# Kernel optimization log

Hardware: AMD Instinct MI355X
Metric: run time of the kernel (lower is better)

Reference implementation:

```python
import jax, jax.numpy as jnp
import numpy as np

B, S, E, H = 4, 2048, 1024, 16
HD = E // H  # head_dim = 64


def setup_inputs() -> dict:
    key = jax.random.key(0)
    ks = jax.random.split(key, 9)
    s_in = 1.0 / np.sqrt(E)
    return {
        "x": jax.random.normal(ks[0], (B, S, E), dtype=jnp.float32),
        "Wq": jax.random.normal(ks[1], (E, E), dtype=jnp.float32) * s_in,
        "bq": jax.random.normal(ks[2], (E,), dtype=jnp.float32) * 0.01,
        "Wk": jax.random.normal(ks[3], (E, E), dtype=jnp.float32) * s_in,
        "bk": jax.random.normal(ks[4], (E,), dtype=jnp.float32) * 0.01,
        "Wv": jax.random.normal(ks[5], (E, E), dtype=jnp.float32) * s_in,
        "bv": jax.random.normal(ks[6], (E,), dtype=jnp.float32) * 0.01,
        "Wo": jax.random.normal(ks[7], (E, E), dtype=jnp.float32) * s_in,
        "bo": jax.random.normal(ks[8], (E,), dtype=jnp.float32) * 0.01,
    }


def reference(x, Wq, bq, Wk, bk, Wv, bv, Wo, bo):
    b, s, e = x.shape
    # fused QKV projections (equivalent to concatenated per-head linears)
    q = x @ Wq + bq  # [b, s, e]
    k = x @ Wk + bk
    v = x @ Wv + bv
    # split heads: [b, h, s, hd]
    def split(t):
        return t.reshape(b, s, H, HD).transpose(0, 2, 1, 3)
    q, k, v = split(q), split(k), split(v)
    scale = 1.0 / np.sqrt(HD)
    attn = jnp.einsum("bhqd,bhkd->bhqk", q, k) * scale  # [b, h, s, s]
    causal = jnp.tril(jnp.ones((s, s), dtype=bool))
    attn = jnp.where(causal[None, None], attn, -jnp.inf)
    attn = jax.nn.softmax(attn, axis=-1)
    y = jnp.einsum("bhqk,bhkd->bhqd", attn, v)  # [b, h, s, hd]
    y = y.transpose(0, 2, 1, 3).reshape(b, s, e)
    return y @ Wo + bo
```

## Files before the change

kernel.cpp:

```cpp
#include <hip/hip_runtime.h>
#include <hip/hip_bf16.h>

#define B_ 4
#define S_ 2048
#define E_ 1024
#define H_ 16
#define HD_ 64
#define QS 3072

typedef __attribute__((ext_vector_type(8))) short bf16x8;
typedef __attribute__((ext_vector_type(4))) float f32x4;

__device__ __forceinline__ float b2f(unsigned short u) {
    union { unsigned u; float f; } v; v.u = ((unsigned)u) << 16; return v.f;
}
__device__ __forceinline__ unsigned short f2b(float f) {
    union { float f; unsigned u; } v; v.f = f;
    unsigned lsb = (v.u >> 16) & 1u;
    v.u += 0x7fffu + lsb;
    return (unsigned short)(v.u >> 16);
}
__device__ __forceinline__ unsigned cvtpk_bf16(float lo, float hi) {
    unsigned r;
    asm("v_cvt_pk_bf16_f32 %0, %1, %2" : "=v"(r) : "v"(lo), "v"(hi));
    return r;
}

typedef const __attribute__((address_space(1))) unsigned glb_u32;
typedef __attribute__((address_space(3))) unsigned lds_u32;
__device__ __forceinline__ void gl_lds16(const unsigned short* g,
                                         unsigned short* l) {
    __builtin_amdgcn_global_load_lds((glb_u32*)g, (lds_u32*)l, 16, 0, 0);
}

__global__ void cvt_f32_to_bf16(const float* __restrict__ in,
                                unsigned short* __restrict__ out, int n8) {
    int i = blockIdx.x * blockDim.x + threadIdx.x;
    if (i >= n8) return;
    const float4* p = (const float4*)(in + (size_t)i * 8);
    float4 a = p[0], b = p[1];
    bf16x8 o;
    o[0] = (short)f2b(a.x); o[1] = (short)f2b(a.y);
    o[2] = (short)f2b(a.z); o[3] = (short)f2b(a.w);
    o[4] = (short)f2b(b.x); o[5] = (short)f2b(b.y);
    o[6] = (short)f2b(b.z); o[7] = (short)f2b(b.w);
    *(bf16x8*)(out + (size_t)i * 8) = o;
}

__global__ void transpose_cvt4(const float* __restrict__ W0,
                               const float* __restrict__ W1,
                               const float* __restrict__ W2,
                               const float* __restrict__ W3,
                               unsigned short* __restrict__ Wqkv,
                               unsigned short* __restrict__ Wto) {
    __shared__ float tile[32][33];
    int z = blockIdx.z;
    const float* W = (z == 0) ? W0 : (z == 1) ? W1 : (z == 2) ? W2 : W3;
    unsigned short* Wt = (z < 3) ? Wqkv + (size_t)z * 1024 * E_ : Wto;
    int tx = threadIdx.x, ty = threadIdx.y;
    int x0 = blockIdx.x * 32, y0 = blockIdx.y * 32;
#pragma unroll
    for (int j = 0; j < 32; j += 8)
        tile[ty + j][tx] = W[(size_t)(y0 + ty + j) * E_ + x0 + tx];
    __syncthreads();
#pragma unroll
    for (int j = 0; j < 32; j += 8)
        Wt[(size_t)(x0 + ty + j) * E_ + y0 + tx] = f2b(tile[tx][ty + j]);
}

#define BM 128
#define BN 128
#define BK 32

__global__ __launch_bounds__(256) void gemm_bt(
        const unsigned short* __restrict__ A,
        const unsigned short* __restrict__ Bt,
        const float* __restrict__ b0, const float* __restrict__ b1,
        const float* __restrict__ b2,
        unsigned short* __restrict__ Cb,
        int M, int N, int K) {
    __shared__ unsigned short As[BM][BK];
    __shared__ unsigned short Bs[BN][BK];
    int t = threadIdx.x;
    int lane = t & 63, wid = t >> 6;
    int wr = wid >> 1, wc = wid & 1;
    int nwg = gridDim.x * gridDim.y;
    int bid = blockIdx.y * gridDim.x + blockIdx.x;
    int ti = (bid & 7) * (nwg >> 3) + (bid >> 3);
    int bx = ti % gridDim.x, by = ti / gridDim.x;
    const int row = t >> 2, kc = (t & 3) << 3;
    const unsigned short* ga0 = A + (size_t)(by * BM + row) * K + kc;
    const unsigned short* gb0 = Bt + (size_t)(bx * BN + row) * K + kc;
    unsigned short* la0 = &As[0][0] + (size_t)t * 8;
    unsigned short* lb0 = &Bs[0][0] + (size_t)t * 8;
    const size_t step64 = (size_t)64 * K;

    f32x4 acc[4][4] = {};

    for (int ko = 0; ko < K; ko += BK) {
        gl_lds16(ga0 + ko, la0);
        gl_lds16(ga0 + ko + step64, la0 + 2048);
        gl_lds16(gb0 + ko, lb0);
        gl_lds16(gb0 + ko + step64, lb0 + 2048);
        __syncthreads();
        int kg = (lane >> 4) << 3;
        bf16x8 af[4], bfr[4];
#pragma unroll
        for (int i = 0; i < 4; ++i) {
            af[i]  = *(const bf16x8*)&As[wr * 64 + i * 16 + (lane & 15)][kg];
            bfr[i] = *(const bf16x8*)&Bs[wc * 64 + i * 16 + (lane & 15)][kg];
        }
#pragma unroll
        for (int i = 0; i < 4; ++i)
#pragma unroll
            for (int j = 0; j < 4; ++j)
                acc[i][j] = __builtin_amdgcn_mfma_f32_16x16x32_bf16(
                    af[i], bfr[j], acc[i][j], 0, 0, 0);
        __syncthreads();
    }

#pragma unroll
    for (int i = 0; i < 4; ++i) {
        int row0 = by * BM + wr * 64 + i * 16 + ((lane >> 4) << 2);
#pragma unroll
        for (int j = 0; j < 4; ++j) {
            int col = bx * BN + wc * 64 + j * 16 + (lane & 15);
            const float* bp = (col < 1024) ? b0 : ((col < 2048) ? b1 : b2);
            float bv = bp[col & 1023];
#pragma unroll
            for (int r = 0; r < 4; ++r) {
                int rr = row0 + r;
                Cb[(size_t)rr * N + col] = f2b(acc[i][j][r] + bv);
            }
        }
    }
}

__global__ __launch_bounds__(256) void gemm_bt_out(
        const unsigned short* __restrict__ A,
        const unsigned short* __restrict__ Bt,
        const float* __restrict__ bias,
        float* __restrict__ Cf, int M, int N, int K) {
    __shared__ unsigned short As[64][BK];
    __shared__ unsigned short Bs[BN][BK];
    int t = threadIdx.x;
    int lane = t & 63, wid = t >> 6;
    int wr = wid >> 1, wc = wid & 1;
    int nwg = gridDim.x * gridDim.y;
    int bid = blockIdx.y * gridDim.x + blockIdx.x;
    int ti = (bid & 7) * (nwg >> 3) + (bid >> 3);
    int bx = ti % gridDim.x, by = ti / gridDim.x;
    const int row = t >> 2, kc = (t & 3) << 3;
    const unsigned short* ga0 = A + (size_t)(by * 64 + row) * K + kc;
    const unsigned short* gb0 = Bt + (size_t)(bx * BN + row) * K + kc;
    unsigned short* la0 = &As[0][0] + (size_t)t * 8;
    unsigned short* lb0 = &Bs[0][0] + (size_t)t * 8;
    const size_t step64 = (size_t)64 * K;

    f32x4 acc[2][4] = {};

    for (int ko = 0; ko < K; ko += BK) {
        gl_lds16(ga0 + ko, la0);
        gl_lds16(gb0 + ko, lb0);
        gl_lds16(gb0 + ko + step64, lb0 + 2048);
        __syncthreads();
        int kg = (lane >> 4) << 3;
        bf16x8 af[2], bfr[4];
#pragma unroll
        for (int i = 0; i < 2; ++i)
            af[i] = *(const bf16x8*)&As[wr * 32 + i * 16 + (lane & 15)][kg];
#pragma unroll
        for (int j = 0; j < 4; ++j)
            bfr[j] = *(const bf16x8*)&Bs[wc * 64 + j * 16 + (lane & 15)][kg];
#pragma unroll
        for (int i = 0; i < 2; ++i)
#pragma unroll
            for (int j = 0; j < 4; ++j)
                acc[i][j] = __builtin_amdgcn_mfma_f32_16x16x32_bf16(
                    af[i], bfr[j], acc[i][j], 0, 0, 0);
        __syncthreads();
    }

#pragma unroll
    for (int i = 0; i < 2; ++i) {
        int row0 = by * 64 + wr * 32 + i * 16 + ((lane >> 4) << 2);
#pragma unroll
        for (int j = 0; j < 4; ++j) {
            int col = bx * BN + wc * 64 + j * 16 + (lane & 15);
            float bv = bias[col];
#pragma unroll
            for (int r = 0; r < 4; ++r)
                Cf[(size_t)(row0 + r) * N + col] = acc[i][j][r] + bv;
        }
    }
}

#define KVBLK 64

__global__ __launch_bounds__(256) void attn_mfma(
        const unsigned short* __restrict__ QKV,
        unsigned short* __restrict__ Yb) {
    __shared__ unsigned short Ks[2][KVBLK][64];
    __shared__ unsigned short Vt[2][64][KVBLK];
    __shared__ unsigned short Pl[4][16][64];

    int t = threadIdx.x;
    int lane = t & 63, wid = t >> 6;
    int l15 = lane & 15, lg = lane >> 4;
    int bh = blockIdx.x;
    int b = bh >> 4, h = bh & 15;
    int by = gridDim.y - 1 - blockIdx.y;
    int qbase = by * 128 + wid * 32;
    int vidx = lg << 4;

    const int kk1 = t >> 3, kk2 = 32 + kk1;
    const int kg1 = ((t & 7) ^ (kk1 & 7)) << 3;
    const int kg2 = ((t & 7) ^ (kk2 & 7)) << 3;
    const int vkey = t >> 2, vc4 = (t & 3) << 4;

    const unsigned short* kvbase = QKV + ((size_t)b * S_) * QS + 1024 + h * 64;

    const float qscale = 0.125f * 1.44269504f;
    bf16x8 qf[2][2];
#pragma unroll
    for (int mt = 0; mt < 2; ++mt)
#pragma unroll
        for (int ks = 0; ks < 2; ++ks) {
            int row = qbase + mt * 16 + l15;
            bf16x8 v = *(const bf16x8*)&QKV[((size_t)(b * S_ + row)) * QS +
                                            h * 64 + ks * 32 + lg * 8];
#pragma unroll
            for (int e = 0; e < 8; ++e)
                qf[mt][ks][e] = (short)f2b(b2f((unsigned short)v[e]) * qscale);
        }

    f32x4 yacc[2][4] = {};
    float m_[2] = {-1e30f, -1e30f}, l_[2] = {0.f, 0.f};

    int ntiles = by * 2 + 2;

    {
        gl_lds16(kvbase + (size_t)kk1 * QS + kg1, &Ks[0][0][0] + (size_t)t * 8);
        gl_lds16(kvbase + (size_t)kk2 * QS + kg2,
                 &Ks[0][0][0] + 2048 + (size_t)t * 8);
        const unsigned short* vsrc = kvbase + 1024 + (size_t)vkey * QS + vc4;
        bf16x8 v0 = *(const bf16x8*)vsrc;
        bf16x8 v1 = *(const bf16x8*)(vsrc + 8);
#pragma unroll
        for (int e = 0; e < 8; ++e) {
            int d0 = vc4 + e, d1 = vc4 + 8 + e;
            int s0 = (d0 & 7) ^ ((d0 >> 3) & 7);
            int s1 = (d1 & 7) ^ ((d1 >> 3) & 7);
            Vt[0][d0][vkey ^ (s0 << 3)] = (unsigned short)v0[e];
            Vt[0][d1][vkey ^ (s1 << 3)] = (unsigned short)v1[e];
        }
    }
    __syncthreads();

    int cur = 0;
    for (int kt = 0; kt < ntiles; ++kt) {
        int k0 = kt * KVBLK;
        bool pre = (kt + 1 < ntiles);
        bf16x8 nv0, nv1;
        if (pre) {
            const unsigned short* kb = kvbase + (size_t)(k0 + KVBLK) * QS;
            unsigned short* ld = &Ks[cur ^ 1][0][0];
            gl_lds16(kb + (size_t)kk1 * QS + kg1, ld + (size_t)t * 8);
            gl_lds16(kb + (size_t)kk2 * QS + kg2, ld + 2048 + (size_t)t * 8);
            const unsigned short* vsrc =
                kb + 1024 + (size_t)vkey * QS + vc4;
            nv0 = *(const bf16x8*)vsrc;
            nv1 = *(const bf16x8*)(vsrc + 8);
        }

        if (k0 <= qbase + 31) {
            bool boundary = (k0 + KVBLK - 1 > qbase);
            f32x4 sacc[2][4] = {};
#pragma unroll
            for (int ks = 0; ks < 2; ++ks) {
                bf16x8 kf[4];
#pragma unroll
                for (int n = 0; n < 4; ++n)
                    kf[n] = *(const bf16x8*)&Ks[cur][n * 16 + l15]
                              [(ks * 32 + lg * 8) ^ ((l15 & 7) << 3)];
#pragma unroll
                for (int mt = 0; mt < 2; ++mt)
#pragma unroll
                    for (int n = 0; n < 4; ++n)
                        sacc[mt][n] = __builtin_amdgcn_mfma_f32_16x16x32_bf16(
                            kf[n], qf[mt][ks], sacc[mt][n], 0, 0, 0);
            }

#pragma unroll
            for (int mt = 0; mt < 2; ++mt) {
                int qv = qbase + mt * 16 + l15;
                if (boundary) {
#pragma unroll
                    for (int n = 0; n < 4; ++n)
#pragma unroll
                        for (int r = 0; r < 4; ++r)
                            if (k0 + n * 16 + lg * 4 + r > qv)
                                sacc[mt][n][r] = -3e38f;
                }
                float pm = -3e38f;
#pragma unroll
                for (int n = 0; n < 4; ++n)
#pragma unroll
                    for (int r = 0; r < 4; ++r)
                        pm = fmaxf(pm, sacc[mt][n][r]);
                pm = fmaxf(pm, __shfl_xor(pm, 16));
                pm = fmaxf(pm, __shfl_xor(pm, 32));
                float mo = m_[mt];
                float mn = mo;
                bool need = __any(pm > mo + 8.0f);
                if (need) {
                    mn = fmaxf(mo, pm);
                    float corr = __builtin_exp2f(mo - mn);
                    m_[mt] = mn;
                    l_[mt] *= corr;
                    int ci = __float_as_int(corr);
#pragma unroll
                    for (int r = 0; r < 4; ++r) {
                        float cq = __int_as_float(
                            __builtin_amdgcn_ds_bpermute(vidx + 4 * r, ci));
#pragma unroll
                        for (int n = 0; n < 4; ++n) yacc[mt][n][r] *= cq;
                    }
                }
                float rs = 0.f;
#pragma unroll
                for (int n = 0; n < 4; ++n)
#pragma unroll
                    for (int r = 0; r < 4; ++r) {
                        float p = __builtin_exp2f(sacc[mt][n][r] - mn);
                        sacc[mt][n][r] = p;
                        rs += p;
                    }
                rs += __shfl_xor(rs, 16);
                rs += __shfl_xor(rs, 32);
                l_[mt] += rs;
#pragma unroll
                for (int n = 0; n < 4; ++n)
#pragma unroll
                    for (int j = 0; j < 2; ++j) {
                        unsigned u = cvtpk_bf16(sacc[mt][n][2 * j],
                                                sacc[mt][n][2 * j + 1]);
                        int col = (n * 16 + lg * 4 + 2 * j) ^ ((l15 & 7) << 3);
                        *(unsigned*)&Pl[wid][l15][col] = u;
                    }
#pragma unroll
                for (int ks = 0; ks < 2; ++ks) {
                    bf16x8 pa, vf[4];
                    pa = *(const bf16x8*)&Pl[wid][l15]
                           [(ks * 32 + lg * 8) ^ ((l15 & 7) << 3)];
#pragma unroll
                    for (int nd = 0; nd < 4; ++nd) {
                        int d = nd * 16 + l15;
                        int sig = (d & 7) ^ ((d >> 3) & 7);
                        vf[nd] = *(const bf16x8*)&Vt[cur][d]
                                   [(ks * 32 + lg * 8) ^ (sig << 3)];
                    }
#pragma unroll
                    for (int nd = 0; nd < 4; ++nd)
                        yacc[mt][nd] = __builtin_amdgcn_mfma_f32_16x16x32_bf16(
                            pa, vf[nd], yacc[mt][nd], 0, 0, 0);
                }
            }
        }

        if (pre) {
#pragma unroll
            for (int e = 0; e < 8; ++e) {
                int d0 = vc4 + e, d1 = vc4 + 8 + e;
                int s0 = (d0 & 7) ^ ((d0 >> 3) & 7);
                int s1 = (d1 & 7) ^ ((d1 >> 3) & 7);
                Vt[cur ^ 1][d0][vkey ^ (s0 << 3)] = (unsigned short)nv0[e];
                Vt[cur ^ 1][d1][vkey ^ (s1 << 3)] = (unsigned short)nv1[e];
            }
        }
        __syncthreads();
        cur ^= 1;
    }

#pragma unroll
    for (int mt = 0; mt < 2; ++mt) {
        float inv = 1.f / l_[mt];
        int ii = __float_as_int(inv);
        float iv[4];
#pragma unroll
        for (int r = 0; r < 4; ++r)
            iv[r] = __int_as_float(
                __builtin_amdgcn_ds_bpermute(vidx + 4 * r, ii));
#pragma unroll
        for (int n = 0; n < 4; ++n)
#pragma unroll
            for (int r = 0; r < 4; ++r) {
                int row = qbase + mt * 16 + lg * 4 + r;
                int d = n * 16 + l15;
                Yb[((size_t)(b * S_ + row)) * E_ + h * 64 + d] =
                    f2b(yacc[mt][n][r] * iv[r]);
            }
    }
}

extern "C" void kernel_launch(void* const* d_in, const int* in_sizes, int n_in,
                              void* d_out, int out_size, void* d_ws, size_t ws_size,
                              hipStream_t stream) {
    const float* x  = (const float*)d_in[0];
    const float* Wq = (const float*)d_in[1];
    const float* bq = (const float*)d_in[2];
    const float* Wk = (const float*)d_in[3];
    const float* bk = (const float*)d_in[4];
    const float* Wv = (const float*)d_in[5];
    const float* bv = (const float*)d_in[6];
    const float* Wo = (const float*)d_in[7];
    const float* bo = (const float*)d_in[8];

    char* ws = (char*)d_ws;
    const size_t M = (size_t)B_ * S_;
    unsigned short* xb   = (unsigned short*)ws;
    unsigned short* QKVb = (unsigned short*)(ws + (16ull << 20));
    unsigned short* Wqkv = (unsigned short*)(ws + (64ull << 20));
    unsigned short* Wto  = (unsigned short*)(ws + (70ull << 20));
    unsigned short* Yb   = xb;

    int n8 = (int)(M * E_ / 8);
    cvt_f32_to_bf16<<<(n8 + 255) / 256, 256, 0, stream>>>(x, xb, n8);

    dim3 tb(32, 8), tg(32, 32, 4);
    transpose_cvt4<<<tg, tb, 0, stream>>>(Wq, Wk, Wv, Wo, Wqkv, Wto);

    dim3 gq(QS / BN, M / BM);
    gemm_bt<<<gq, 256, 0, stream>>>(xb, Wqkv, bq, bk, bv, QKVb,
                                    (int)M, QS, E_);

    dim3 ag(B_ * H_, S_ / 128);
    attn_mfma<<<ag, 256, 0, stream>>>(QKVb, Yb);

    dim3 gg(E_ / BN, M / 64);
    gemm_bt_out<<<gg, 256, 0, stream>>>(Yb, Wto, bo, (float*)d_out,
                                        (int)M, E_, E_);
}
```

Before: 207.3 us.

## Pair complementary causal query tiles per block for balanced attention work

Each attention block now processes two 64-row query tiles (qt = 31-y and qt = y) in sequence, so every block does the same total causal work. Each wave now handles 16 query rows instead of 32, which halves the per-wave accumulator state. The trade-off is that K/V tiles are no longer shared across as many query rows, so K/V loads from global memory go up. The first K/V tile of the second pass is also reloaded serially, adding a pipeline restart.

```diff
diff --git a/kernel.cpp b/kernel.cpp
--- a/kernel.cpp
+++ b/kernel.cpp
@@ -209,122 +209,121 @@
     int l15 = lane & 15, lg = lane >> 4;
     int bh = blockIdx.x;
     int b = bh >> 4, h = bh & 15;
-    int by = gridDim.y - 1 - blockIdx.y;
-    int qbase = by * 128 + wid * 32;
     int vidx = lg << 4;
 
     const int kk1 = t >> 3, kk2 = 32 + kk1;
     const int kg1 = ((t & 7) ^ (kk1 & 7)) << 3;
     const int kg2 = ((t & 7) ^ (kk2 & 7)) << 3;
     const int vkey = t >> 2, vc4 = (t & 3) << 4;
+    const float qscale = 0.125f * 1.44269504f;
 
     const unsigned short* kvbase = QKV + ((size_t)b * S_) * QS + 1024 + h * 64;
 
-    const float qscale = 0.125f * 1.44269504f;
-    bf16x8 qf[2][2];
-#pragma unroll
-    for (int mt = 0; mt < 2; ++mt)
+    int cur = 0;
+#pragma unroll 1
+    for (int uu = 0; uu < 2; ++uu) {
+        int qt = uu ? blockIdx.y : (31 - blockIdx.y);
+        int qbase = qt * 64 + wid * 16;
+
+        bf16x8 qf[2];
 #pragma unroll
         for (int ks = 0; ks < 2; ++ks) {
-            int row = qbase + mt * 16 + l15;
+            int row = qbase + l15;
             bf16x8 v = *(const bf16x8*)&QKV[((size_t)(b * S_ + row)) * QS +
                                             h * 64 + ks * 32 + lg * 8];
 #pragma unroll
             for (int e = 0; e < 8; ++e)
-                qf[mt][ks][e] = (short)f2b(b2f((unsigned short)v[e]) * qscale);
-        }
-
-    f32x4 yacc[2][4] = {};
-    float m_[2] = {-1e30f, -1e30f}, l_[2] = {0.f, 0.f};
-
-    int ntiles = by * 2 + 2;
-
-    {
-        gl_lds16(kvbase + (size_t)kk1 * QS + kg1, &Ks[0][0][0] + (size_t)t * 8);
-        gl_lds16(kvbase + (size_t)kk2 * QS + kg2,
-                 &Ks[0][0][0] + 2048 + (size_t)t * 8);
-        const unsigned short* vsrc = kvbase + 1024 + (size_t)vkey * QS + vc4;
-        bf16x8 v0 = *(const bf16x8*)vsrc;
-        bf16x8 v1 = *(const bf16x8*)(vsrc + 8);
-#pragma unroll
-        for (int e = 0; e < 8; ++e) {
-            int d0 = vc4 + e, d1 = vc4 + 8 + e;
-            int s0 = (d0 & 7) ^ ((d0 >> 3) & 7);
-            int s1 = (d1 & 7) ^ ((d1 >> 3) & 7);
-            Vt[0][d0][vkey ^ (s0 << 3)] = (unsigned short)v0[e];
-            Vt[0][d1][vkey ^ (s1 << 3)] = (unsigned short)v1[e];
-        }
-    }
-    __syncthreads();
-
-    int cur = 0;
-    for (int kt = 0; kt < ntiles; ++kt) {
-        int k0 = kt * KVBLK;
-        bool pre = (kt + 1 < ntiles);
-        bf16x8 nv0, nv1;
-        if (pre) {
-            const unsigned short* kb = kvbase + (size_t)(k0 + KVBLK) * QS;
-            unsigned short* ld = &Ks[cur ^ 1][0][0];
-            gl_lds16(kb + (size_t)kk1 * QS + kg1, ld + (size_t)t * 8);
-            gl_lds16(kb + (size_t)kk2 * QS + kg2, ld + 2048 + (size_t)t * 8);
+                qf[ks][e] = (short)f2b(b2f((unsigned short)v[e]) * qscale);
+        }
+
+        f32x4 yacc[4] = {};
+        float m_ = -1e30f, l_ = 0.f;
+        int ntiles = qt + 1;
+
+        {
+            gl_lds16(kvbase + (size_t)kk1 * QS + kg1,
+                     &Ks[cur][0][0] + (size_t)t * 8);
+            gl_lds16(kvbase + (size_t)kk2 * QS + kg2,
+                     &Ks[cur][0][0] + 2048 + (size_t)t * 8);
             const unsigned short* vsrc =
-                kb + 1024 + (size_t)vkey * QS + vc4;
-            nv0 = *(const bf16x8*)vsrc;
-            nv1 = *(const bf16x8*)(vsrc + 8);
-        }
-
-        if (k0 <= qbase + 31) {
-            bool boundary = (k0 + KVBLK - 1 > qbase);
-            f32x4 sacc[2][4] = {};
-#pragma unroll
-            for (int ks = 0; ks < 2; ++ks) {
-                bf16x8 kf[4];
-#pragma unroll
-                for (int n = 0; n < 4; ++n)
-                    kf[n] = *(const bf16x8*)&Ks[cur][n * 16 + l15]
-                              [(ks * 32 + lg * 8) ^ ((l15 & 7) << 3)];
-#pragma unroll
-                for (int mt = 0; mt < 2; ++mt)
+                kvbase + 1024 + (size_t)vkey * QS + vc4;
+            bf16x8 v0 = *(const bf16x8*)vsrc;
+            bf16x8 v1 = *(const bf16x8*)(vsrc + 8);
+#pragma unroll
+            for (int e = 0; e < 8; ++e) {
+                int d0 = vc4 + e, d1 = vc4 + 8 + e;
+                int s0 = (d0 & 7) ^ ((d0 >> 3) & 7);
+                int s1 = (d1 & 7) ^ ((d1 >> 3) & 7);
+                Vt[cur][d0][vkey ^ (s0 << 3)] = (unsigned short)v0[e];
+                Vt[cur][d1][vkey ^ (s1 << 3)] = (unsigned short)v1[e];
+            }
+        }
+        __syncthreads();
+
+        for (int kt = 0; kt < ntiles; ++kt) {
+            int k0 = kt * KVBLK;
+            bool pre = (kt + 1 < ntiles);
+            bf16x8 nv0, nv1;
+            if (pre) {
+                const unsigned short* kb = kvbase + (size_t)(k0 + KVBLK) * QS;
+                unsigned short* ld = &Ks[cur ^ 1][0][0];
+                gl_lds16(kb + (size_t)kk1 * QS + kg1, ld + (size_t)t * 8);
+                gl_lds16(kb + (size_t)kk2 * QS + kg2,
+                         ld + 2048 + (size_t)t * 8);
+                const unsigned short* vsrc =
+                    kb + 1024 + (size_t)vkey * QS + vc4;
+                nv0 = *(const bf16x8*)vsrc;
+                nv1 = *(const bf16x8*)(vsrc + 8);
+            }
+
+            if (k0 <= qbase + 15) {
+                bool boundary = (k0 + KVBLK - 1 > qbase);
+                f32x4 sacc[4] = {};
+#pragma unroll
+                for (int ks = 0; ks < 2; ++ks) {
+                    bf16x8 kf[4];
 #pragma unroll
                     for (int n = 0; n < 4; ++n)
-                        sacc[mt][n] = __builtin_amdgcn_mfma_f32_16x16x32_bf16(
-                            kf[n], qf[mt][ks], sacc[mt][n], 0, 0, 0);
-            }
-
-#pragma unroll
-            for (int mt = 0; mt < 2; ++mt) {
-                int qv = qbase + mt * 16 + l15;
+                        kf[n] = *(const bf16x8*)&Ks[cur][n * 16 + l15]
+                                  [(ks * 32 + lg * 8) ^ ((l15 & 7) << 3)];
+#pragma unroll
+                    for (int n = 0; n < 4; ++n)
+                        sacc[n] = __builtin_amdgcn_mfma_f32_16x16x32_bf16(
+                            kf[n], qf[ks], sacc[n], 0, 0, 0);
+                }
+
+                int qv = qbase + l15;
                 if (boundary) {
 #pragma unroll
                     for (int n = 0; n < 4; ++n)
 #pragma unroll
                         for (int r = 0; r < 4; ++r)
                             if (k0 + n * 16 + lg * 4 + r > qv)
-                                sacc[mt][n][r] = -3e38f;
+                                sacc[n][r] = -3e38f;
                 }
                 float pm = -3e38f;
 #pragma unroll
                 for (int n = 0; n < 4; ++n)
 #pragma unroll
                     for (int r = 0; r < 4; ++r)
-                        pm = fmaxf(pm, sacc[mt][n][r]);
+                        pm = fmaxf(pm, sacc[n][r]);
                 pm = fmaxf(pm, __shfl_xor(pm, 16));
                 pm = fmaxf(pm, __shfl_xor(pm, 32));
-                float mo = m_[mt];
+                float mo = m_;
                 float mn = mo;
                 bool need = __any(pm > mo + 8.0f);
                 if (need) {
                     mn = fmaxf(mo, pm);
                     float corr = __builtin_exp2f(mo - mn);
-                    m_[mt] = mn;
-                    l_[mt] *= corr;
+                    m_ = mn;
+                    l_ *= corr;
                     int ci = __float_as_int(corr);
 #pragma unroll
                     for (int r = 0; r < 4; ++r) {
                         float cq = __int_as_float(
                             __builtin_amdgcn_ds_bpermute(vidx + 4 * r, ci));
 #pragma unroll
-                        for (int n = 0; n < 4; ++n) yacc[mt][n][r] *= cq;
+                        for (int n = 0; n < 4; ++n) yacc[n][r] *= cq;
                     }
                 }
                 float rs = 0.f;
@@ -332,19 +331,19 @@
                 for (int n = 0; n < 4; ++n)
 #pragma unroll
                     for (int r = 0; r < 4; ++r) {
-                        float p = __builtin_exp2f(sacc[mt][n][r] - mn);
-                        sacc[mt][n][r] = p;
+                        float p = __builtin_exp2f(sacc[n][r] - mn);
+                        sacc[n][r] = p;
                         rs += p;
                     }
                 rs += __shfl_xor(rs, 16);
                 rs += __shfl_xor(rs, 32);
-                l_[mt] += rs;
+                l_ += rs;
 #pragma unroll
                 for (int n = 0; n < 4; ++n)
 #pragma unroll
                     for (int j = 0; j < 2; ++j) {
-                        unsigned u = cvtpk_bf16(sacc[mt][n][2 * j],
-                                                sacc[mt][n][2 * j + 1]);
+                        unsigned u = cvtpk_bf16(sacc[n][2 * j],
+                                                sacc[n][2 * j + 1]);
                         int col = (n * 16 + lg * 4 + 2 * j) ^ ((l15 & 7) << 3);
                         *(unsigned*)&Pl[wid][l15][col] = u;
                     }
@@ -362,44 +361,43 @@
                     }
 #pragma unroll
                     for (int nd = 0; nd < 4; ++nd)
-                        yacc[mt][nd] = __builtin_amdgcn_mfma_f32_16x16x32_bf16(
-                            pa, vf[nd], yacc[mt][nd], 0, 0, 0);
+                        yacc[nd] = __builtin_amdgcn_mfma_f32_16x16x32_bf16(
+                            pa, vf[nd], yacc[nd], 0, 0, 0);
                 }
             }
-        }
-
-        if (pre) {
-#pragma unroll
-            for (int e = 0; e < 8; ++e) {
-                int d0 = vc4 + e, d1 = vc4 + 8 + e;
-                int s0 = (d0 & 7) ^ ((d0 >> 3) & 7);
-                int s1 = (d1 & 7) ^ ((d1 >> 3) & 7);
-                Vt[cur ^ 1][d0][vkey ^ (s0 << 3)] = (unsigned short)nv0[e];
-                Vt[cur ^ 1][d1][vkey ^ (s1 << 3)] = (unsigned short)nv1[e];
+
+            if (pre) {
+#pragma unroll
+                for (int e = 0; e < 8; ++e) {
+                    int d0 = vc4 + e, d1 = vc4 + 8 + e;
+                    int s0 = (d0 & 7) ^ ((d0 >> 3) & 7);
+                    int s1 = (d1 & 7) ^ ((d1 >> 3) & 7);
+                    Vt[cur ^ 1][d0][vkey ^ (s0 << 3)] = (unsigned short)nv0[e];
+                    Vt[cur ^ 1][d1][vkey ^ (s1 << 3)] = (unsigned short)nv1[e];
+                }
             }
-        }
-        __syncthreads();
-        cur ^= 1;
-    }
-
-#pragma unroll
-    for (int mt = 0; mt < 2; ++mt) {
-        float inv = 1.f / l_[mt];
-        int ii = __float_as_int(inv);
-        float iv[4];
-#pragma unroll
-        for (int r = 0; r < 4; ++r)
-            iv[r] = __int_as_float(
-                __builtin_amdgcn_ds_bpermute(vidx + 4 * r, ii));
-#pragma unroll
-        for (int n = 0; n < 4; ++n)
-#pragma unroll
-            for (int r = 0; r < 4; ++r) {
-                int row = qbase + mt * 16 + lg * 4 + r;
-                int d = n * 16 + l15;
-                Yb[((size_t)(b * S_ + row)) * E_ + h * 64 + d] =
-                    f2b(yacc[mt][n][r] * iv[r]);
-            }
+            __syncthreads();
+            cur ^= 1;
+        }
+
+        {
+            float inv = 1.f / l_;
+            int ii = __float_as_int(inv);
+            float iv[4];
+#pragma unroll
+            for (int r = 0; r < 4; ++r)
+                iv[r] = __int_as_float(
+                    __builtin_amdgcn_ds_bpermute(vidx + 4 * r, ii));
+#pragma unroll
+            for (int n = 0; n < 4; ++n)
+#pragma unroll
+                for (int r = 0; r < 4; ++r) {
+                    int row = qbase + lg * 4 + r;
+                    int d = n * 16 + l15;
+                    Yb[((size_t)(b * S_ + row)) * E_ + h * 64 + d] =
+                        f2b(yacc[n][r] * iv[r]);
+                }
+        }
     }
 }
 
@@ -434,7 +432,7 @@
     gemm_bt<<<gq, 256, 0, stream>>>(xb, Wqkv, bq, bk, bv, QKVb,
                                     (int)M, QS, E_);
 
-    dim3 ag(B_ * H_, S_ / 128);
+    dim3 ag(B_ * H_, 16);
     attn_mfma<<<ag, 256, 0, stream>>>(QKVb, Yb);
 
     dim3 gg(E_ / BN, M / 64);
```

After: 222.1 us. 7.1% more time.

## Pack V transpose stores as key pairs, defer row-sum reduce, add MFMA priority

Applied to the files above, without the earlier changes.

The V tile is now loaded as two consecutive key rows of eight dims per thread. Each pair is written into the transposed LDS buffer as a packed 32-bit store, replacing the 16-bit scattered stores. The per-tile cross-lane reduction of the softmax row sum is moved to the end, which is valid because the running correction factor is uniform across those lanes. s_setprio is raised around the MFMA blocks to favour matrix issue among waves. The packed stores cut LDS store count, at the cost of a different bank pattern for the swizzled writes.

```diff
diff --git a/kernel.cpp b/kernel.cpp
--- a/kernel.cpp
+++ b/kernel.cpp
@@ -216,7 +216,9 @@
     const int kk1 = t >> 3, kk2 = 32 + kk1;
     const int kg1 = ((t & 7) ^ (kk1 & 7)) << 3;
     const int kg2 = ((t & 7) ^ (kk2 & 7)) << 3;
-    const int vkey = t >> 2, vc4 = (t & 3) << 4;
+    const int vp2 = (t >> 3) << 1;
+    const int vdc = t & 7;
+    const int vd0 = vdc << 3;
 
     const unsigned short* kvbase = QKV + ((size_t)b * S_) * QS + 1024 + h * 64;
 
@@ -243,16 +245,16 @@
         gl_lds16(kvbase + (size_t)kk1 * QS + kg1, &Ks[0][0][0] + (size_t)t * 8);
         gl_lds16(kvbase + (size_t)kk2 * QS + kg2,
                  &Ks[0][0][0] + 2048 + (size_t)t * 8);
-        const unsigned short* vsrc = kvbase + 1024 + (size_t)vkey * QS + vc4;
+        const unsigned short* vsrc = kvbase + 1024 + (size_t)vp2 * QS + vd0;
         bf16x8 v0 = *(const bf16x8*)vsrc;
-        bf16x8 v1 = *(const bf16x8*)(vsrc + 8);
+        bf16x8 v1 = *(const bf16x8*)(vsrc + QS);
 #pragma unroll
         for (int e = 0; e < 8; ++e) {
-            int d0 = vc4 + e, d1 = vc4 + 8 + e;
-            int s0 = (d0 & 7) ^ ((d0 >> 3) & 7);
-            int s1 = (d1 & 7) ^ ((d1 >> 3) & 7);
-            Vt[0][d0][vkey ^ (s0 << 3)] = (unsigned short)v0[e];
-            Vt[0][d1][vkey ^ (s1 << 3)] = (unsigned short)v1[e];
+            int d = vd0 + e;
+            int sig = e ^ vdc;
+            unsigned u = (unsigned)(unsigned short)v0[e] |
+                         ((unsigned)(unsigned short)v1[e] << 16);
+            *(unsigned*)&Vt[0][d][vp2 ^ (sig << 3)] = u;
         }
     }
     __syncthreads();
@@ -267,15 +269,15 @@
             unsigned short* ld = &Ks[cur ^ 1][0][0];
             gl_lds16(kb + (size_t)kk1 * QS + kg1, ld + (size_t)t * 8);
             gl_lds16(kb + (size_t)kk2 * QS + kg2, ld + 2048 + (size_t)t * 8);
-            const unsigned short* vsrc =
-                kb + 1024 + (size_t)vkey * QS + vc4;
+            const unsigned short* vsrc = kb + 1024 + (size_t)vp2 * QS + vd0;
             nv0 = *(const bf16x8*)vsrc;
-            nv1 = *(const bf16x8*)(vsrc + 8);
+            nv1 = *(const bf16x8*)(vsrc + QS);
         }
 
         if (k0 <= qbase + 31) {
             bool boundary = (k0 + KVBLK - 1 > qbase);
             f32x4 sacc[2][4] = {};
+            __builtin_amdgcn_s_setprio(1);
 #pragma unroll
             for (int ks = 0; ks < 2; ++ks) {
                 bf16x8 kf[4];
@@ -290,6 +292,7 @@
                         sacc[mt][n] = __builtin_amdgcn_mfma_f32_16x16x32_bf16(
                             kf[n], qf[mt][ks], sacc[mt][n], 0, 0, 0);
             }
+            __builtin_amdgcn_s_setprio(0);
 
 #pragma unroll
             for (int mt = 0; mt < 2; ++mt) {
@@ -336,8 +339,6 @@
                         sacc[mt][n][r] = p;
                         rs += p;
                     }
-                rs += __shfl_xor(rs, 16);
-                rs += __shfl_xor(rs, 32);
                 l_[mt] += rs;
 #pragma unroll
                 for (int n = 0; n < 4; ++n)
@@ -348,6 +349,7 @@
                         int col = (n * 16 + lg * 4 + 2 * j) ^ ((l15 & 7) << 3);
                         *(unsigned*)&Pl[wid][l15][col] = u;
                     }
+                __builtin_amdgcn_s_setprio(1);
 #pragma unroll
                 for (int ks = 0; ks < 2; ++ks) {
                     bf16x8 pa, vf[4];
@@ -365,17 +367,18 @@
                         yacc[mt][nd] = __builtin_amdgcn_mfma_f32_16x16x32_bf16(
                             pa, vf[nd], yacc[mt][nd], 0, 0, 0);
                 }
+                __builtin_amdgcn_s_setprio(0);
             }
         }
 
         if (pre) {
 #pragma unroll
             for (int e = 0; e < 8; ++e) {
-                int d0 = vc4 + e, d1 = vc4 + 8 + e;
-                int s0 = (d0 & 7) ^ ((d0 >> 3) & 7);
-                int s1 = (d1 & 7) ^ ((d1 >> 3) & 7);
-                Vt[cur ^ 1][d0][vkey ^ (s0 << 3)] = (unsigned short)nv0[e];
-                Vt[cur ^ 1][d1][vkey ^ (s1 << 3)] = (unsigned short)nv1[e];
+                int d = vd0 + e;
+                int sig = e ^ vdc;
+                unsigned u = (unsigned)(unsigned short)nv0[e] |
+                             ((unsigned)(unsigned short)nv1[e] << 16);
+                *(unsigned*)&Vt[cur ^ 1][d][vp2 ^ (sig << 3)] = u;
             }
         }
         __syncthreads();
@@ -384,7 +387,10 @@
 
 #pragma unroll
     for (int mt = 0; mt < 2; ++mt) {
-        float inv = 1.f / l_[mt];
+        float lt = l_[mt];
+        lt += __shfl_xor(lt, 16);
+        lt += __shfl_xor(lt, 32);
+        float inv = 1.f / lt;
         int ii = __float_as_int(inv);
         float iv[4];
 #pragma unroll
```

New measurement: 209.2 us. Within noise of the previous version (+0.9%).
